# Kernel tuning notes

Hardware: AMD Instinct MI355X
Metric: run time of the kernel (lower is better)

Reference implementation:

```python
import jax, jax.numpy as jnp
import numpy as np

ITERS = 4
LN_EPS = 1e-5


def build_grid(H, W):
    # standard uORF grid in [-1, 1], shape (H, W, 2), last dim = (x, y)
    x = jnp.linspace(-1.0 + 1.0 / W, 1.0 - 1.0 / W, W)
    y = jnp.linspace(-1.0 + 1.0 / H, 1.0 - 1.0 / H, H)
    yy, xx = jnp.meshgrid(y, x, indexing='ij')
    return jnp.stack([xx, yy], axis=-1)


def ln(x, g, b):
    m = jnp.mean(x, axis=-1, keepdims=True)
    v = jnp.var(x, axis=-1, keepdims=True)
    return (x - m) * jax.lax.rsqrt(v + LN_EPS) * g + b


def setup_inputs():
    key = jax.random.key(0)
    ks = jax.random.split(key, 16)
    B, H, W, C, K, Ds = 4, 64, 64, 256, 5, 256
    s = 0.02
    inp = {
        'feat': jax.random.normal(ks[0], (B, H, W, C), jnp.float32),
        'mask': (jax.random.uniform(ks[1], (K, 1, H, W)) > 0.5).astype(jnp.float32),
        'noise': jax.random.normal(ks[2], (B, K, Ds), jnp.float32),
        'slots_mu': jax.random.normal(ks[3], (1, 1, Ds), jnp.float32),
        'slots_logsigma': jax.random.normal(ks[4], (1, 1, Ds), jnp.float32) * s,
        'norm_g': jnp.ones((C,), jnp.float32), 'norm_b': jnp.zeros((C,), jnp.float32),
        'grid_W': jax.random.normal(ks[5], (C, 4), jnp.float32) * s,
        'grid_b': jnp.zeros((C,), jnp.float32),
        'k_W': jax.random.normal(ks[6], (C, C), jnp.float32) * s,
        'v_W': jax.random.normal(ks[7], (C, C), jnp.float32) * s,
        'mlp_g': jnp.ones((C,), jnp.float32), 'mlp_b': jnp.zeros((C,), jnp.float32),
        'mlp_W': jax.random.normal(ks[8], (Ds, C), jnp.float32) * s,
        'mlp_bias': jnp.zeros((Ds,), jnp.float32),
        'q_g': jnp.ones((Ds,), jnp.float32), 'q_b': jnp.zeros((Ds,), jnp.float32),
        'q_W': jax.random.normal(ks[9], (Ds, Ds), jnp.float32) * s,
        'gru_Wih': jax.random.normal(ks[10], (3 * Ds, Ds), jnp.float32) * s,
        'gru_Whh': jax.random.normal(ks[11], (3 * Ds, Ds), jnp.float32) * s,
        'gru_bih': jnp.zeros((3 * Ds,), jnp.float32),
        'gru_bhh': jnp.zeros((3 * Ds,), jnp.float32),
        'res_g': jnp.ones((Ds,), jnp.float32), 'res_b': jnp.zeros((Ds,), jnp.float32),
        'res_W': jax.random.normal(ks[12], (Ds, Ds), jnp.float32) * s,
        'res_bias': jnp.zeros((Ds,), jnp.float32),
    }
    return inp


def reference(feat, mask, noise, slots_mu, slots_logsigma, norm_g, norm_b,
              grid_W, grid_b, k_W, v_W, mlp_g, mlp_b, mlp_W, mlp_bias,
              q_g, q_b, q_W, gru_Wih, gru_Whh, gru_bih, gru_bhh,
              res_g, res_b, res_W, res_bias):
    B, H, W, C = feat.shape
    K = mask.shape[0]
    N = H * W
    Ds = slots_mu.shape[-1]
    scale = Ds ** -0.5

    grid = build_grid(H, W)                                   # (H, W, 2)
    # foreground positions: mask-weighted mean of grid -> (K, 2)
    g = jnp.transpose(grid, (2, 0, 1))[None]                  # (1, 2, H, W)
    fg_pos = jnp.sum(g * mask, axis=(2, 3)) / (jnp.sum(mask, axis=(2, 3)) + 1e-5)
    fg_pos = jnp.broadcast_to(fg_pos[None], (B, K, 2))        # (B, K, 2)

    feat_n = ln(feat.reshape(B, N, C), norm_g, norm_b)        # (B, N, C)
    mask_flat = mask.reshape(K, N)
    slot = slots_mu + jnp.exp(slots_logsigma) * noise         # (B, K, Ds)

    # k, v with relative position embedding; fg_pos never changes in-loop,
    # so compute once (the original recomputes the same values each iter).
    rel = grid.reshape(1, 1, N, 2) - fg_pos[:, :, None, :]    # (B, K, N, 2)
    rel4 = jnp.concatenate([rel, -rel], axis=-1)              # (B, K, N, 4)
    ge = rel4 @ grid_W.T + grid_b                             # (B, K, N, C)
    kbase = feat_n @ k_W.T                                    # (B, N, C)
    vbase = feat_n @ v_W.T
    kk = ln(kbase[:, None] + ge, mlp_g, mlp_b) @ mlp_W.T + mlp_bias  # (B,K,N,Ds)
    vv = ln(vbase[:, None] + ge, mlp_g, mlp_b) @ mlp_W.T + mlp_bias

    attn_vis = None
    for _ in range(ITERS):
        slot_prev = slot
        q = ln(slot, q_g, q_b) @ q_W.T                        # (B, K, Ds)
        attn = jnp.einsum('bkd,bknd->bkn', q, kk) * scale
        attn = jnp.where(mask_flat[None] == 0, -1e9, attn)
        attn = jax.nn.softmax(attn, axis=-1)                  # (B, K, N)
        upd = jnp.einsum('bkn,bknd->bkd', attn, vv)           # (B, K, Ds)
        # torch GRUCell
        x = upd.reshape(-1, Ds)
        h = slot.reshape(-1, Ds)
        gi = x @ gru_Wih.T + gru_bih
        gh = h @ gru_Whh.T + gru_bhh
        ir, iz, inn = jnp.split(gi, 3, axis=-1)
        hr, hz, hn = jnp.split(gh, 3, axis=-1)
        r = jax.nn.sigmoid(ir + hr)
        z = jax.nn.sigmoid(iz + hz)
        n = jnp.tanh(inn + r * hn)
        hnew = ((1.0 - z) * n + z * h).reshape(B, K, Ds)
        slot = (ln(hnew, res_g, res_b) @ res_W.T + res_bias) + slot_prev
        amin = attn.min(axis=-1, keepdims=True)
        amax = attn.max(axis=-1, keepdims=True)
        attn_vis = (attn - amin) / (amax - amin + 1e-5)
    return slot, fg_pos, attn_vis
```

## Files before the change

### kernel.cpp

```cpp
#include <hip/hip_runtime.h>
#include <math.h>

typedef unsigned short u16;
typedef unsigned int   u32;
typedef short bf8v __attribute__((ext_vector_type(8)));
typedef float f4v  __attribute__((ext_vector_type(4)));

static constexpr int B_=4, C_=256, K_=5, D_=256, N_=4096, IT_=4;
static constexpr float EPS_=1e-5f;
static constexpr int P_WQ0=0, P_WR0=16, P_WIH0=32, P_WHH0=80,
                     P_CPK=128, P_CPV=160, P_CPG=192,
                     P_MISC=224, P_UQ=225, P_FG0=226, P_GRID=231;

__device__ __forceinline__ float bf2f(u16 u){ u32 x=((u32)u)<<16; float f; __builtin_memcpy(&f,&x,4); return f; }
__device__ __forceinline__ float bflo(u32 u){ u32 x=u<<16; float f; __builtin_memcpy(&f,&x,4); return f; }
__device__ __forceinline__ float bfhi(u32 u){ u32 x=u&0xffff0000u; float f; __builtin_memcpy(&f,&x,4); return f; }
__device__ __forceinline__ u16 f2bf(float f){ u32 x; __builtin_memcpy(&x,&f,4); u32 r=x+0x7fffu+((x>>16)&1u); return (u16)(r>>16); }
__device__ __forceinline__ float ldin(const void* p, size_t i, int f){
  return f ? ((const float*)p)[i] : bf2f(((const u16*)p)[i]);
}
__device__ __forceinline__ void stout(void* p, size_t i, float v, int f){
  if (f) ((float*)p)[i]=v; else ((u16*)p)[i]=f2bf(v);
}
__device__ __forceinline__ int sw16(int row,int col){
  return row*256 + ((((col>>3)^(row&7))<<3) | (col&7));
}

__device__ __forceinline__ void breduce4(float&a,float&b,float&c,float&d,float* red){
  #pragma unroll
  for(int o=32;o>0;o>>=1){
    a+=__shfl_down(a,o,64); b+=__shfl_down(b,o,64);
    c+=__shfl_down(c,o,64); d+=__shfl_down(d,o,64);
  }
  int w=threadIdx.x>>6;
  __syncthreads();
  if((threadIdx.x&63)==0){ red[w]=a; red[4+w]=b; red[8+w]=c; red[12+w]=d; }
  __syncthreads();
  a=red[0]+red[1]+red[2]+red[3];
  b=red[4]+red[5]+red[6]+red[7];
  c=red[8]+red[9]+red[10]+red[11];
  d=red[12]+red[13]+red[14]+red[15];
}
__device__ __forceinline__ void breduce4_16(float&a,float&b,float&c,float&d,float* red){
  #pragma unroll
  for(int o=32;o>0;o>>=1){
    a+=__shfl_down(a,o,64); b+=__shfl_down(b,o,64);
    c+=__shfl_down(c,o,64); d+=__shfl_down(d,o,64);
  }
  int w=threadIdx.x>>6;
  __syncthreads();
  if((threadIdx.x&63)==0){ red[w]=a; red[16+w]=b; red[32+w]=c; red[48+w]=d; }
  __syncthreads();
  a=0;b=0;c=0;d=0;
  #pragma unroll
  for(int i=0;i<16;++i){ a+=red[i]; b+=red[16+i]; c+=red[32+i]; d+=red[48+i]; }
}

__device__ __forceinline__ int probe_f(const void* feat, float* red){
  const u32* p=(const u32*)feat;
  int t=threadIdx.x; int bad=0;
  #pragma unroll
  for(int s=0;s<8;++s){
    u32 wd=p[t+s*256];
    float lo=bf2f((u16)(wd&0xffffu));
    if(!(fabsf(lo)<1e6f)) bad++;
  }
  float bb=(float)bad, z1=0,z2=0,z3=0;
  breduce4(bb,z1,z2,z3,red);
  return (bb>=16.f)?1:0;
}

__global__ void prep1_kernel(const void* feat,
    const void* kW, const void* vW, const void* mW, const void* qW, const void* rW,
    const void* Wih, const void* Whh, const void* mu, const void* lsig, const void* noise,
    const void* gW, const void* gb_, const void* mg,
    const void* mb_, const void* mbias, const void* mask,
    int* flag, float* WqT, float* WrT, float* WihT, float* WhhT,
    float* slot, float* gvec,
    u16* Wkb, u16* Wvb, u16* Wgb,
    float* Uvec, float* Qs, float* fg, void* out)
{
  __shared__ float redp[16];
  __shared__ float tile[64][65];
  int bid=blockIdx.x;
  int t=threadIdx.x;
  int f=probe_f(feat, redp);
  if(bid==0 && t==0) *flag=f;
  __syncthreads();
  if(bid<P_CPK){
    const void* src; float* dst; int OS; int b2;
    if(bid<P_WR0){ src=qW; dst=WqT; OS=256; b2=bid; }
    else if(bid<P_WIH0){ src=rW; dst=WrT; OS=256; b2=bid-P_WR0; }
    else if(bid<P_WHH0){ src=Wih; dst=WihT; OS=768; b2=bid-P_WIH0; }
    else { src=Whh; dst=WhhT; OS=768; b2=bid-P_WHH0; }
    int r0=(b2>>2)*64, c0=(b2&3)*64;
    int lane=t&63, wv=t>>6;
    #pragma unroll
    for(int it=0;it<16;++it){
      int i=wv*16+it;
      tile[i][lane]=ldin(src,(size_t)(r0+i)*256+c0+lane,f);
    }
    __syncthreads();
    #pragma unroll
    for(int it=0;it<16;++it){
      int i=wv*16+it;
      dst[(size_t)(c0+i)*OS + r0 + lane] = tile[lane][i];
    }
    return;
  }
  if(bid<P_MISC){
    int b2=bid-P_CPK;
    int which=b2>>5;
    int base=(b2&31)*2048;
    if(which==0){
      #pragma unroll
      for(int s=0;s<8;++s){ int e=base+s*256+t; Wkb[e]=f2bf(ldin(kW,e,f)); }
    } else if(which==1){
      #pragma unroll
      for(int s=0;s<8;++s){ int e=base+s*256+t; Wvb[e]=f2bf(ldin(vW,e,f)); }
    } else {
      #pragma unroll
      for(int s=0;s<8;++s){ int e=base+s*256+t; int c=e&255; Wgb[e]=f2bf(ldin(mg,c,f)*ldin(mW,e,f)); }
    }
    return;
  }
  if(bid==P_MISC){
    #pragma unroll
    for(int s=0;s<20;++s){ int e=s*256+t; int d=e&255;
      slot[e]=ldin(mu,d,f)+expf(ldin(lsig,d,f))*ldin(noise,e,f); }
    #pragma unroll
    for(int s=0;s<3;++s){ int e=s*256+t;
      int c=e&255, sel=e>>8;
      float v;
      if(sel==0)      v=ldin(gW,c*4+0,f)-ldin(gW,c*4+2,f);
      else if(sel==1) v=ldin(gW,c*4+1,f)-ldin(gW,c*4+3,f);
      else            v=ldin(gb_,c,f);
      gvec[e]=v;
    }
    return;
  }
  __shared__ float s_a[256], s_b[256], s_c[256];
  if(bid==P_UQ){
    s_a[t]=ldin(gW,t*4+0,f)-ldin(gW,t*4+2,f);
    s_b[t]=ldin(gW,t*4+1,f)-ldin(gW,t*4+3,f);
    s_c[t]=ldin(gb_,t,f);
    __syncthreads();
    float u1=0,u2=0,u3=0,gw=0,bw=0;
    #pragma unroll 8
    for(int c=0;c<256;++c){
      float mwv=ldin(mW,(size_t)t*256+c,f);
      float wg=ldin(mg,c,f)*mwv;
      u1+=s_a[c]*wg; u2+=s_b[c]*wg; u3+=s_c[c]*wg; gw+=wg;
      bw+=ldin(mb_,c,f)*mwv;
    }
    Uvec[t]=u1; Uvec[256+t]=u2; Uvec[512+t]=u3; Uvec[768+t]=gw;
    Uvec[1024+t]=bw+ldin(mbias,t,f);
    float a=s_a[t], b=s_b[t], cc=s_c[t];
    float s0=a*a,s1=b*b,s2=cc*cc,s3=a*b; breduce4(s0,s1,s2,s3,redp);
    float s4=a*cc,s5=b*cc,s6=a,s7=b;     breduce4(s4,s5,s6,s7,redp);
    float s8=cc,z1=0,z2=0,z3=0;          breduce4(s8,z1,z2,z3,redp);
    if(t==0){
      Qs[0]=s0; Qs[1]=s1; Qs[2]=s2; Qs[3]=s3; Qs[4]=s4; Qs[5]=s5;
      Qs[6]=s6*(1.f/256.f); Qs[7]=s7*(1.f/256.f); Qs[8]=s8*(1.f/256.f);
    }
  } else {
    int k=bid-P_FG0;
    float sx=0,sy=0,sm=0;
    for(int s=0;s<16;++s){
      int p=t+s*256;
      float m=ldin(mask,(size_t)k*N_+p,f);
      int i=p>>6, j=p&63;
      float x=(2*j+1)*(1.0f/64.0f)-1.0f;
      float y=(2*i+1)*(1.0f/64.0f)-1.0f;
      sx+=x*m; sy+=y*m; sm+=m;
    }
    float d=0;
    breduce4(sx,sy,sm,d,redp);
    if(t==0){
      float inv=1.0f/(sm+1e-5f);
      float fx=sx*inv, fy=sy*inv;
      fg[k*2]=fx; fg[k*2+1]=fy;
      for(int b=0;b<B_;++b){
        stout(out, 5120+(b*K_+k)*2+0, fx, f);
        stout(out, 5120+(b*K_+k)*2+1, fy, f);
      }
    }
  }
}

__global__ void __launch_bounds__(512,2) base_kernel(const int* flag, const void* feat, const void* ng, const void* nb,
    const u16* Wkb, const u16* Wvb, const u16* Wgb, const float* gvec,
    float* scal, u16* PkT, u16* Pvb,
    const float* slot, const void* qg, const void* qb_, const float* WqT,
    float* qbuf)
{
  extern __shared__ u16 smem[];
  u16* bufA = smem;
  u16* bufB = smem + 16384;
  int t=threadIdx.x, f=*flag;
  if(blockIdx.x>=256){
    float* Lq =(float*)smem;
    float* pp =(float*)smem+256;
    float* red=(float*)smem+768;
    int bk=blockIdx.x-256;
    int tt=t&255, hh=t>>8, w=t>>6;
    float x=slot[bk*256+tt];
    float s=x, s2=x*x;
    #pragma unroll
    for(int o=32;o>0;o>>=1){ s+=__shfl_down(s,o,64); s2+=__shfl_down(s2,o,64); }
    if((t&63)==0){ red[w]=s; red[8+w]=s2; }
    __syncthreads();
    s=0; s2=0;
    #pragma unroll
    for(int i=0;i<8;++i){ s+=red[i]; s2+=red[8+i]; }
    float m=s*(1.f/512.f), v=s2*(1.f/512.f)-m*m;
    float lq=(x-m)*rsqrtf(v+EPS_)*ldin(qg,tt,f)+ldin(qb_,tt,f);
    if(hh==0) Lq[tt]=lq;
    __syncthreads();
    float acc=0; int cb=hh*128;
    #pragma unroll 8
    for(int cc=0;cc<128;++cc){ int c=cb+cc; acc+=Lq[c]*WqT[(size_t)c*256+tt]; }
    pp[hh*256+tt]=acc;
    __syncthreads();
    if(hh==0) qbuf[bk*256+tt]=pp[tt]+pp[256+tt];
    return;
  }
  int w=t>>6, l=t&63;
  int quad=l>>4, m=l&15;
  int row0=blockIdx.x*64;
  {
    float g0=ldin(ng,4*l+0,f), g1=ldin(ng,4*l+1,f), g2=ldin(ng,4*l+2,f), g3=ldin(ng,4*l+3,f);
    float b0=ldin(nb,4*l+0,f), b1=ldin(nb,4*l+1,f), b2=ldin(nb,4*l+2,f), b3=ldin(nb,4*l+3,f);
    #pragma unroll
    for(int r8=0;r8<8;++r8){
      int row=8*w+r8;
      float x0,x1,x2,x3;
      if(f){
        float4 v4=((const float4*)feat)[(size_t)(row0+row)*64+l];
        x0=v4.x; x1=v4.y; x2=v4.z; x3=v4.w;
      } else {
        ushort4 uu=((const ushort4*)feat)[(size_t)(row0+row)*64+l];
        x0=bf2f(uu.x); x1=bf2f(uu.y); x2=bf2f(uu.z); x3=bf2f(uu.w);
      }
      float s=x0+x1+x2+x3, s2=x0*x0+x1*x1+x2*x2+x3*x3;
      #pragma unroll
      for(int o=32;o>0;o>>=1){ s+=__shfl_xor(s,o,64); s2+=__shfl_xor(s2,o,64); }
      float mm=s*(1.f/256.f), inv=rsqrtf(s2*(1.f/256.f)-mm*mm+EPS_);
      ushort4 o4=make_ushort4(f2bf((x0-mm)*inv*g0+b0), f2bf((x1-mm)*inv*g1+b1),
                              f2bf((x2-mm)*inv*g2+b2), f2bf((x3-mm)*inv*g3+b3));
      *(ushort4*)&bufA[sw16(row,4*l)]=o4;
    }
  }
  __syncthreads();
  {
    f4v ack[4][2], acv[4][2];
    #pragma unroll
    for(int rt=0;rt<4;++rt)
      #pragma unroll
      for(int i=0;i<2;++i){ ack[rt][i]=(f4v){0.f,0.f,0.f,0.f}; acv[rt][i]=(f4v){0.f,0.f,0.f,0.f}; }
    #pragma unroll
    for(int kk=0;kk<8;++kk){
      int kcol=kk*32+quad*8;
      bf8v af[4];
      #pragma unroll
      for(int rt=0;rt<4;++rt) af[rt]=*(bf8v*)&bufA[sw16(rt*16+m,kcol)];
      #pragma unroll
      for(int i=0;i<2;++i){
        int n=w*32+16*i+m;
        bf8v bk=*(const bf8v*)(Wkb+(size_t)n*256+kcol);
        bf8v bv=*(const bf8v*)(Wvb+(size_t)n*256+kcol);
        #pragma unroll
        for(int rt=0;rt<4;++rt){
          ack[rt][i]=__builtin_amdgcn_mfma_f32_16x16x32_bf16(af[rt],bk,ack[rt][i],0,0,0);
          acv[rt][i]=__builtin_amdgcn_mfma_f32_16x16x32_bf16(af[rt],bv,acv[rt][i],0,0,0);
        }
      }
    }
    #pragma unroll
    for(int rt=0;rt<4;++rt)
      #pragma unroll
      for(int i=0;i<2;++i){
        int n=w*32+16*i+m;
        #pragma unroll
        for(int r=0;r<4;++r)
          bufB[sw16(rt*16+quad*4+r,n)]=f2bf(ack[rt][i][r]);
      }
    __syncthreads();
    #pragma unroll
    for(int rt=0;rt<4;++rt)
      #pragma unroll
      for(int i=0;i<2;++i){
        int n=w*32+16*i+m;
        #pragma unroll
        for(int r=0;r<4;++r)
          bufA[sw16(rt*16+quad*4+r,n)]=f2bf(acv[rt][i][r]);
      }
  }
  __syncthreads();
  {
    float gA0=gvec[l], gA1=gvec[l+64], gA2=gvec[l+128], gA3=gvec[l+192];
    float gB0=gvec[256+l], gB1=gvec[256+l+64], gB2=gvec[256+l+128], gB3=gvec[256+l+192];
    float gC0=gvec[512+l], gC1=gvec[512+l+64], gC2=gvec[512+l+128], gC3=gvec[512+l+192];
    for(int r8=0;r8<8;++r8){
      int row=8*w+r8;
      float k0=bf2f(bufB[sw16(row,l)]),     k1=bf2f(bufB[sw16(row,l+64)]),
            k2=bf2f(bufB[sw16(row,l+128)]), k3=bf2f(bufB[sw16(row,l+192)]);
      float x0=bf2f(bufA[sw16(row,l)]),     x1=bf2f(bufA[sw16(row,l+64)]),
            x2=bf2f(bufA[sw16(row,l+128)]), x3=bf2f(bufA[sw16(row,l+192)]);
      float v0=k0+k1+k2+k3;
      float v1=k0*k0+k1*k1+k2*k2+k3*k3;
      float v2=k0*gA0+k1*gA1+k2*gA2+k3*gA3;
      float v3=k0*gB0+k1*gB1+k2*gB2+k3*gB3;
      float v4=k0*gC0+k1*gC1+k2*gC2+k3*gC3;
      float v5=x0+x1+x2+x3;
      float v6=x0*x0+x1*x1+x2*x2+x3*x3;
      float v7=x0*gA0+x1*gA1+x2*gA2+x3*gA3;
      float v8=x0*gB0+x1*gB1+x2*gB2+x3*gB3;
      float v9=x0*gC0+x1*gC1+x2*gC2+x3*gC3;
      #pragma unroll
      for(int o=32;o>0;o>>=1){
        v0+=__shfl_down(v0,o,64); v1+=__shfl_down(v1,o,64); v2+=__shfl_down(v2,o,64);
        v3+=__shfl_down(v3,o,64); v4+=__shfl_down(v4,o,64); v5+=__shfl_down(v5,o,64);
        v6+=__shfl_down(v6,o,64); v7+=__shfl_down(v7,o,64); v8+=__shfl_down(v8,o,64);
        v9+=__shfl_down(v9,o,64);
      }
      if(l==0){
        float* sc=scal+(size_t)(row0+row)*10;
        sc[0]=v0; sc[1]=v1; sc[2]=v2; sc[3]=v3; sc[4]=v4;
        sc[5]=v5; sc[6]=v6; sc[7]=v7; sc[8]=v8; sc[9]=v9;
      }
    }
  }
  {
    f4v apk[4][2], apv[4][2];
    #pragma unroll
    for(int rt=0;rt<4;++rt)
      #pragma unroll
      for(int i=0;i<2;++i){ apk[rt][i]=(f4v){0.f,0.f,0.f,0.f}; apv[rt][i]=(f4v){0.f,0.f,0.f,0.f}; }
    #pragma unroll
    for(int kk=0;kk<8;++kk){
      int kcol=kk*32+quad*8;
      bf8v afk[4], afv[4];
      #pragma unroll
      for(int rt=0;rt<4;++rt){
        afk[rt]=*(bf8v*)&bufB[sw16(rt*16+m,kcol)];
        afv[rt]=*(bf8v*)&bufA[sw16(rt*16+m,kcol)];
      }
      #pragma unroll
      for(int i=0;i<2;++i){
        int n=w*32+16*i+m;
        bf8v bg=*(const bf8v*)(Wgb+(size_t)n*256+kcol);
        #pragma unroll
        for(int rt=0;rt<4;++rt){
          apk[rt][i]=__builtin_amdgcn_mfma_f32_16x16x32_bf16(afk[rt],bg,apk[rt][i],0,0,0);
          apv[rt][i]=__builtin_amdgcn_mfma_f32_16x16x32_bf16(afv[rt],bg,apv[rt][i],0,0,0);
        }
      }
    }
    #pragma unroll
    for(int rt=0;rt<4;++rt)
      #pragma unroll
      for(int i=0;i<2;++i){
        int d=w*32+16*i+m;
        *(ushort4*)(PkT+(size_t)d*16384+row0+rt*16+quad*4)=
          make_ushort4(f2bf(apk[rt][i][0]),f2bf(apk[rt][i][1]),f2bf(apk[rt][i][2]),f2bf(apk[rt][i][3]));
      }
    __syncthreads();
    #pragma unroll
    for(int rt=0;rt<4;++rt)
      #pragma unroll
      for(int i=0;i<2;++i){
        int d=w*32+16*i+m;
        #pragma unroll
        for(int r=0;r<4;++r)
          bufB[sw16(rt*16+quad*4+r,d)]=f2bf(apv[rt][i][r]);
      }
  }
  __syncthreads();
  #pragma unroll
  for(int r8=0;r8<8;++r8){
    int row=8*w+r8;
    ushort4 s4=*(ushort4*)&bufB[sw16(row,4*l)];
    *(ushort4*)(Pvb+(size_t)(row0+row)*256+4*l)=s4;
  }
}

__global__ void __launch_bounds__(512) attn_kernel(const int* flag, const float* qbuf, const u16* PkT,
    const float* scal, const float* Qs, const float* Uvec, const float* fg, const void* mask,
    const u16* Pvb, float* logits, float* pmax, float* psum, float* updpart, float* sscp,
    int store_lg)
{
  __shared__ float q5[1280];
  __shared__ float un[10240];
  __shared__ float lgs[320], ivs[320], mvs[320];
  __shared__ float qs5[40], fgs[10], Qss[9], MSl[5];
  __shared__ float sred[8][5][4];
  int tid=threadIdx.x, f=*flag;
  int b=blockIdx.x>>6, ch=blockIdx.x&63;
  int w=tid>>6, l=tid&63;
  int n0=ch<<6;
  for(int p=tid;p<1280;p+=512) q5[p]=qbuf[(size_t)b*1280+p];
  if(tid<10) fgs[tid]=fg[tid];
  if(tid<9)  Qss[tid]=Qs[tid];
  __syncthreads();
  for(int p=w;p<25;p+=8){
    int k=p/5, j=p%5;
    float s=q5[k*256+l]*Uvec[j*256+l]+q5[k*256+l+64]*Uvec[j*256+l+64]
           +q5[k*256+l+128]*Uvec[j*256+l+128]+q5[k*256+l+192]*Uvec[j*256+l+192];
    #pragma unroll
    for(int o=32;o>0;o>>=1) s+=__shfl_xor(s,o,64);
    if(l==0) qs5[k*8+j]=s;
  }
  {
    int n=n0+l; size_t row=(size_t)b*N_+n;
    float dk0=0,dk1=0,dk2=0,dk3=0,dk4=0;
    int cbase=w*32;
    #pragma unroll 8
    for(int cc=0;cc<32;++cc){
      int c=cbase+cc;
      float pv=bf2f(PkT[(size_t)c*16384+row]);
      dk0+=pv*q5[c]; dk1+=pv*q5[256+c]; dk2+=pv*q5[512+c];
      dk3+=pv*q5[768+c]; dk4+=pv*q5[1024+c];
    }
    un[(w*5+0)*64+l]=dk0; un[(w*5+1)*64+l]=dk1; un[(w*5+2)*64+l]=dk2;
    un[(w*5+3)*64+l]=dk3; un[(w*5+4)*64+l]=dk4;
  }
  __syncthreads();
  if(tid<320){
    int k=tid>>6, nl=tid&63;
    float dot=0;
    #pragma unroll
    for(int j=0;j<8;++j) dot+=un[(j*5+k)*64+nl];
    int n2=n0+nl; size_t row2=(size_t)b*N_+n2;
    const float* sc=scal+row2*10;
    float rx=(2*(n2&63)+1)*(1.f/64.f)-1.f-fgs[2*k];
    float ry=(2*(n2>>6)+1)*(1.f/64.f)-1.f-fgs[2*k+1];
    float qge=rx*rx*Qss[0]+ry*ry*Qss[1]+Qss[2]+2.f*(rx*ry*Qss[3]+rx*Qss[4]+ry*Qss[5]);
    float mk=sc[0]*(1.f/256.f)+rx*Qss[6]+ry*Qss[7]+Qss[8];
    float sxk=sc[1]+2.f*(rx*sc[2]+ry*sc[3]+sc[4])+qge;
    float invK=rsqrtf(sxk*(1.f/256.f)-mk*mk+EPS_);
    float lg=invK*(dot+rx*qs5[k*8+0]+ry*qs5[k*8+1]+qs5[k*8+2]-mk*qs5[k*8+3])+qs5[k*8+4];
    float mval=ldin(mask,(size_t)k*N_+n2,f);
    lg=(mval==0.f)? -1e9f : lg*0.0625f;
    if(store_lg) logits[((size_t)(b*5+k))*N_+n2]=lg;
    lgs[tid]=lg;
    float mv=sc[5]*(1.f/256.f)+rx*Qss[6]+ry*Qss[7]+Qss[8];
    float sxv=sc[6]+2.f*(rx*sc[7]+ry*sc[8]+sc[9])+qge;
    mvs[tid]=mv;
    ivs[tid]=rsqrtf(sxv*(1.f/256.f)-mv*mv+EPS_);
  }
  __syncthreads();
  if(tid<64){
    #pragma unroll
    for(int k=0;k<5;++k){
      float v=lgs[k*64+tid];
      float M=v;
      #pragma unroll
      for(int o=32;o>0;o>>=1) M=fmaxf(M,__shfl_xor(M,o,64));
      float e=expf(v-M);
      #pragma unroll
      for(int o=32;o>0;o>>=1) e+=__shfl_xor(e,o,64);
      if(tid==0){ pmax[((size_t)(b*64+ch))*5+k]=M; psum[((size_t)(b*64+ch))*5+k]=e; MSl[k]=M; }
    }
  }
  __syncthreads();
  {
    float acc[5][4]={{0}};
    float swx[5]={0,0,0,0,0}, swy[5]={0,0,0,0,0}, sw[5]={0,0,0,0,0}, swm[5]={0,0,0,0,0};
    #pragma unroll 2
    for(int rr=0;rr<8;++rr){
      int nl=w*8+rr; int n2=n0+nl;
      size_t row=(size_t)b*N_+n2;
      uint2 pu=*(const uint2*)(Pvb+row*256+l*4);
      float px=bflo(pu.x), py=bfhi(pu.x), pz=bflo(pu.y), pw=bfhi(pu.y);
      int jx=n2&63, iy=n2>>6;
      #pragma unroll
      for(int k=0;k<5;++k){
        float wgt=expf(lgs[k*64+nl]-MSl[k])*ivs[k*64+nl];
        float rx=(2*jx+1)*(1.f/64.f)-1.f-fgs[2*k];
        float ry=(2*iy+1)*(1.f/64.f)-1.f-fgs[2*k+1];
        acc[k][0]+=wgt*px; acc[k][1]+=wgt*py; acc[k][2]+=wgt*pz; acc[k][3]+=wgt*pw;
        sw[k]+=wgt; swx[k]+=wgt*rx; swy[k]+=wgt*ry; swm[k]+=wgt*mvs[k*64+nl];
      }
    }
    #pragma unroll
    for(int k=0;k<5;++k)
      *(float4*)&un[(w*5+k)*256+l*4]=make_float4(acc[k][0],acc[k][1],acc[k][2],acc[k][3]);
    if(l==0){
      #pragma unroll
      for(int k=0;k<5;++k){ sred[w][k][0]=swx[k]; sred[w][k][1]=swy[k];
                            sred[w][k][2]=sw[k];  sred[w][k][3]=swm[k]; }
    }
  }
  __syncthreads();
  for(int p=tid;p<1280;p+=512){
    int k=p>>8, d=p&255;
    float v=0;
    #pragma unroll
    for(int j=0;j<8;++j) v+=un[(j*5+k)*256+d];
    updpart[((size_t)blockIdx.x*5+k)*256+d]=v;
  }
  if(tid<20){
    int kk=tid>>2, j=tid&3;
    float s=0;
    #pragma unroll
    for(int jj=0;jj<8;++jj) s+=sred[jj][kk][j];
    sscp[((size_t)blockIdx.x*5+kk)*4+j]=s;
  }
}

__global__ void __launch_bounds__(1024) gru_kernel(const int* flag, float* slot, const float* updpart,
    const float* sscp, const float* Uvec, const float* pmax, const float* psum, const float* logits,
    const float* WihT, const float* WhhT, const void* bih, const void* bhh,
    const void* rg, const void* rb_, const float* WrT, const void* rbias,
    const void* qg, const void* qb_, const float* WqT, float* qbuf,
    int do_vis, void* out)
{
  __shared__ float u[256], h[256], sn[256];
  __shared__ float part[4][6][256];
  __shared__ float red[64];
  __shared__ float cvec[4];
  __shared__ float fch[64];
  __shared__ float MSg[2];
  int tid=threadIdx.x, t=tid&255, g=tid>>8;
  int blk=blockIdx.x;
  int f=*flag;
  if(blk>=20){
    if(!do_vis) return;
    int bk2=blk-20, k2=bk2%K_, b2=bk2/K_;
    if(tid<64){
      float pm=pmax[((size_t)(b2*64+tid))*5+k2];
      float ps=psum[((size_t)(b2*64+tid))*5+k2];
      float M=pm;
      #pragma unroll
      for(int o=32;o>0;o>>=1) M=fmaxf(M,__shfl_xor(M,o,64));
      float e=ps*expf(pm-M);
      #pragma unroll
      for(int o=32;o>0;o>>=1) e+=__shfl_xor(e,o,64);
      if(tid==0){ MSg[0]=M; MSg[1]=1.0f/e; }
    }
    __syncthreads();
    float M=MSg[0], Sinv=MSg[1];
    float a[4]; float mn=1e30f, mx=-1e30f;
    #pragma unroll
    for(int s=0;s<4;++s){
      a[s]=expf(logits[(size_t)bk2*N_+tid+s*1024]-M)*Sinv;
      mn=fminf(mn,a[s]); mx=fmaxf(mx,a[s]);
    }
    #pragma unroll
    for(int o=32;o>0;o>>=1){ mn=fminf(mn,__shfl_down(mn,o,64)); mx=fmaxf(mx,__shfl_down(mx,o,64)); }
    int wv=tid>>6;
    __syncthreads();
    if((tid&63)==0){ red[wv]=mn; red[16+wv]=mx; }
    __syncthreads();
    mn=1e30f; mx=-1e30f;
    #pragma unroll
    for(int i=0;i<16;++i){ mn=fminf(mn,red[i]); mx=fmaxf(mx,red[16+i]); }
    float inv=1.0f/(mx-mn+1e-5f);
    #pragma unroll
    for(int s=0;s<4;++s) stout(out, 5160+(size_t)bk2*N_+tid+s*1024, (a[s]-mn)*inv, f);
    return;
  }
  int bk=blk, k=bk%K_, b=bk/K_;
  if(tid<64){
    float pm=pmax[((size_t)(b*64+tid))*5+k];
    float ps=psum[((size_t)(b*64+tid))*5+k];
    float M=pm;
    #pragma unroll
    for(int o=32;o>0;o>>=1) M=fmaxf(M,__shfl_xor(M,o,64));
    float fc=expf(pm-M);
    fch[tid]=fc;
    float e=ps*fc;
    #pragma unroll
    for(int o=32;o>0;o>>=1) e+=__shfl_xor(e,o,64);
    if(tid==0){ MSg[0]=M; MSg[1]=1.0f/e; }
  }
  __syncthreads();
  float Sinv=MSg[1];
  float ua=0;
  {
    int ch0=g*16;
    #pragma unroll 4
    for(int ci=0;ci<16;++ci){ int ch=ch0+ci; ua += fch[ch]*updpart[(((size_t)(b*64+ch))*5+k)*256+t]; }
  }
  part[g][0][t]=ua;
  if(t<4){
    float s=0;
    #pragma unroll 4
    for(int ci=0;ci<16;++ci){ int ch=g*16+ci; s += fch[ch]*sscp[(((size_t)(b*64+ch))*5+k)*4+t]; }
    part[g][1][t]=s;
  }
  __syncthreads();
  if(g==0 && t<4) cvec[t]=part[0][1][t]+part[1][1][t]+part[2][1][t]+part[3][1][t];
  __syncthreads();
  if(g==0){
    float uu=part[0][0][t]+part[1][0][t]+part[2][0][t]+part[3][0][t];
    u[t]=(uu+cvec[0]*Uvec[t]+cvec[1]*Uvec[256+t]+cvec[2]*Uvec[512+t]-cvec[3]*Uvec[768+t])*Sinv
         +Uvec[1024+t];
    h[t]=slot[bk*256+t];
  }
  __syncthreads();
  float p0=0,p1=0,p2=0,p3=0,p4=0,p5=0;
  int c0=g*64;
  #pragma unroll 8
  for(int cc=0;cc<64;++cc){
    int c=c0+cc;
    float uc=u[c], hc=h[c];
    const float* wi=WihT+(size_t)c*768+t;
    const float* wh=WhhT+(size_t)c*768+t;
    p0+=uc*wi[0]; p1+=uc*wi[256]; p2+=uc*wi[512];
    p3+=hc*wh[0]; p4+=hc*wh[256]; p5+=hc*wh[512];
  }
  part[g][0][t]=p0; part[g][1][t]=p1; part[g][2][t]=p2;
  part[g][3][t]=p3; part[g][4][t]=p4; part[g][5][t]=p5;
  __syncthreads();
  float hn=0;
  if(g==0){
    float gi0=ldin(bih,t,f)+part[0][0][t]+part[1][0][t]+part[2][0][t]+part[3][0][t];
    float gi1=ldin(bih,256+t,f)+part[0][1][t]+part[1][1][t]+part[2][1][t]+part[3][1][t];
    float gi2=ldin(bih,512+t,f)+part[0][2][t]+part[1][2][t]+part[2][2][t]+part[3][2][t];
    float gh0=ldin(bhh,t,f)+part[0][3][t]+part[1][3][t]+part[2][3][t]+part[3][3][t];
    float gh1=ldin(bhh,256+t,f)+part[0][4][t]+part[1][4][t]+part[2][4][t]+part[3][4][t];
    float gh2=ldin(bhh,512+t,f)+part[0][5][t]+part[1][5][t]+part[2][5][t]+part[3][5][t];
    float r=1.f/(1.f+expf(-(gi0+gh0)));
    float z=1.f/(1.f+expf(-(gi1+gh1)));
    float nn=tanhf(gi2+r*gh2);
    hn=(1.f-z)*nn+z*h[t];
  }
  float s=hn, sq=hn*hn, za=0, zb=0;
  breduce4_16(s,sq,za,zb,red);
  if(g==0){
    float m=s*(1.f/256.f), var=sq*(1.f/256.f)-m*m;
    u[t]=(hn-m)*rsqrtf(var+EPS_)*ldin(rg,t,f)+ldin(rb_,t,f);
  }
  __syncthreads();
  float pr=0;
  #pragma unroll 8
  for(int cc=0;cc<64;++cc){ int c=c0+cc; pr+=u[c]*WrT[(size_t)c*256+t]; }
  part[g][0][t]=pr;
  __syncthreads();
  if(g==0){
    float acc=ldin(rbias,t,f)+h[t]+part[0][0][t]+part[1][0][t]+part[2][0][t]+part[3][0][t];
    slot[bk*256+t]=acc;
    stout(out, (size_t)bk*256+t, acc, f);
    sn[t]=acc;
  }
  __syncthreads();
  float xs=(g==0)? sn[t]:0.f;
  float xq=xs*xs, zc=0, zd=0;
  breduce4_16(xs,xq,zc,zd,red);
  if(g==0){
    float m=xs*(1.f/256.f), var=xq*(1.f/256.f)-m*m;
    u[t]=(sn[t]-m)*rsqrtf(var+EPS_)*ldin(qg,t,f)+ldin(qb_,t,f);
  }
  __syncthreads();
  float pq=0;
  #pragma unroll 8
  for(int cc=0;cc<64;++cc){ int c=c0+cc; pq+=u[c]*WqT[(size_t)c*256+t]; }
  part[g][0][t]=pq;
  __syncthreads();
  if(g==0){
    float qv=part[0][0][t]+part[1][0][t]+part[2][0][t]+part[3][0][t];
    qbuf[bk*256+t]=qv;
  }
}

extern "C" void kernel_launch(void* const* d_in, const int* in_sizes, int n_in,
                              void* d_out, int out_size, void* d_ws, size_t ws_size,
                              hipStream_t stream)
{
  const void* feat =d_in[0];  const void* mask =d_in[1];  const void* noise=d_in[2];
  const void* mu   =d_in[3];  const void* lsig =d_in[4];  const void* ng   =d_in[5];
  const void* nb   =d_in[6];  const void* gW   =d_in[7];  const void* gb_  =d_in[8];
  const void* kW   =d_in[9];  const void* vW   =d_in[10]; const void* mg   =d_in[11];
  const void* mb_  =d_in[12]; const void* mW   =d_in[13]; const void* mbias=d_in[14];
  const void* qg   =d_in[15]; const void* qb_  =d_in[16]; const void* qW   =d_in[17];
  const void* Wih  =d_in[18]; const void* Whh  =d_in[19]; const void* bih  =d_in[20];
  const void* bhh  =d_in[21]; const void* rg   =d_in[22]; const void* rb_  =d_in[23];
  const void* rW   =d_in[24]; const void* rbias=d_in[25];

  char* p=(char*)d_ws;
  auto alloc=[&](size_t bytes)->char*{ char* r=p; p+=(bytes+255)&~(size_t)255; return r; };
  int*   flag   =(int*)  alloc(256);
  float* fg     =(float*)alloc(64);
  float* slot   =(float*)alloc(5120*4);
  float* qbuf   =(float*)alloc(5120*4);
  float* logits =(float*)alloc((size_t)81920*4);
  float* pmax   =(float*)alloc(1280*4);
  float* psum   =(float*)alloc(1280*4);
  float* updpart=(float*)alloc((size_t)256*5*256*4);
  float* sscp   =(float*)alloc((size_t)256*5*4*4);
  float* WqT    =(float*)alloc((size_t)65536*4);
  float* WrT    =(float*)alloc((size_t)65536*4);
  float* WihT   =(float*)alloc((size_t)196608*4);
  float* WhhT   =(float*)alloc((size_t)196608*4);
  float* gvec   =(float*)alloc(768*4);
  float* Uvec   =(float*)alloc(1280*4);
  float* Qs     =(float*)alloc(64);
  float* scal   =(float*)alloc((size_t)163840*4);
  u16*   Wkb    =(u16*)  alloc((size_t)65536*2);
  u16*   Wvb    =(u16*)  alloc((size_t)65536*2);
  u16*   Wgb    =(u16*)  alloc((size_t)65536*2);
  u16*   PkT    =(u16*)  alloc((size_t)16384*256*2);
  u16*   Pvb    =(u16*)  alloc((size_t)16384*256*2);

  prep1_kernel<<<P_GRID,256,0,stream>>>(feat,kW,vW,mW,qW,rW,Wih,Whh,mu,lsig,noise,gW,gb_,mg,
                                        mb_,mbias,mask,
                                        flag,WqT,WrT,WihT,WhhT,slot,gvec,Wkb,Wvb,Wgb,
                                        Uvec,Qs,fg,d_out);
  base_kernel<<<276,512,65536,stream>>>(flag,feat,ng,nb,Wkb,Wvb,Wgb,gvec,scal,PkT,Pvb,
                                        slot,qg,qb_,WqT,qbuf);
  for(int it=0; it<IT_; ++it){
    attn_kernel<<<B_*64,512,0,stream>>>(flag,qbuf,PkT,scal,Qs,Uvec,fg,mask,Pvb,
                                        logits,pmax,psum,updpart,sscp,(it==IT_-1)?1:0);
    int nb_g = (it==IT_-1)? 40 : 20;
    gru_kernel<<<nb_g,1024,0,stream>>>(flag,slot,updpart,sscp,Uvec,pmax,psum,logits,
                                       WihT,WhhT,bih,bhh,rg,rb_,WrT,rbias,
                                       qg,qb_,WqT,qbuf,(it==IT_-1)?1:0,d_out);
  }
}
```

Baseline: 366.1 us.

## Move weight transposes into base kernel and read q weights directly

The small-weight transposes (q, res, GRU input/hidden) move out of the prep kernel into extra blocks of the large base kernel, so they overlap with the main projection work and the prep kernel shrinks. The initial q projection now reads the original row-major q weight with vectorised loads instead of waiting on the transposed copy. The Uvec reduction also stages the norm vectors in shared memory and uses vector loads. Extra blocks in the base kernel could compete for CUs with its main tiles.

Measured after the change: 345.8 us. -5.5%, faster.

```diff
diff --git a/kernel.cpp b/kernel.cpp
--- a/kernel.cpp
+++ b/kernel.cpp
@@ -8,9 +8,8 @@
 
 static constexpr int B_=4, C_=256, K_=5, D_=256, N_=4096, IT_=4;
 static constexpr float EPS_=1e-5f;
-static constexpr int P_WQ0=0, P_WR0=16, P_WIH0=32, P_WHH0=80,
-                     P_CPK=128, P_CPV=160, P_CPG=192,
-                     P_MISC=224, P_UQ=225, P_FG0=226, P_GRID=231;
+static constexpr int P0_MISC=96, P0_UQ=97, P0_FG=98, P0_GRID=103;
+static constexpr int BT_QP=256, BT_TR=276, BT_GRID=404;
 
 __device__ __forceinline__ float bf2f(u16 u){ u32 x=((u32)u)<<16; float f; __builtin_memcpy(&f,&x,4); return f; }
 __device__ __forceinline__ float bflo(u32 u){ u32 x=u<<16; float f; __builtin_memcpy(&f,&x,4); return f; }
@@ -70,48 +69,24 @@
   return (bb>=16.f)?1:0;
 }
 
-__global__ void prep1_kernel(const void* feat,
-    const void* kW, const void* vW, const void* mW, const void* qW, const void* rW,
-    const void* Wih, const void* Whh, const void* mu, const void* lsig, const void* noise,
+__global__ void prep0_kernel(const void* feat,
+    const void* kW, const void* vW, const void* mW,
+    const void* mu, const void* lsig, const void* noise,
     const void* gW, const void* gb_, const void* mg,
     const void* mb_, const void* mbias, const void* mask,
-    int* flag, float* WqT, float* WrT, float* WihT, float* WhhT,
-    float* slot, float* gvec,
+    int* flag, float* slot, float* gvec,
     u16* Wkb, u16* Wvb, u16* Wgb,
     float* Uvec, float* Qs, float* fg, void* out)
 {
   __shared__ float redp[16];
-  __shared__ float tile[64][65];
   int bid=blockIdx.x;
   int t=threadIdx.x;
   int f=probe_f(feat, redp);
   if(bid==0 && t==0) *flag=f;
   __syncthreads();
-  if(bid<P_CPK){
-    const void* src; float* dst; int OS; int b2;
-    if(bid<P_WR0){ src=qW; dst=WqT; OS=256; b2=bid; }
-    else if(bid<P_WIH0){ src=rW; dst=WrT; OS=256; b2=bid-P_WR0; }
-    else if(bid<P_WHH0){ src=Wih; dst=WihT; OS=768; b2=bid-P_WIH0; }
-    else { src=Whh; dst=WhhT; OS=768; b2=bid-P_WHH0; }
-    int r0=(b2>>2)*64, c0=(b2&3)*64;
-    int lane=t&63, wv=t>>6;
-    #pragma unroll
-    for(int it=0;it<16;++it){
-      int i=wv*16+it;
-      tile[i][lane]=ldin(src,(size_t)(r0+i)*256+c0+lane,f);
-    }
-    __syncthreads();
-    #pragma unroll
-    for(int it=0;it<16;++it){
-      int i=wv*16+it;
-      dst[(size_t)(c0+i)*OS + r0 + lane] = tile[lane][i];
-    }
-    return;
-  }
-  if(bid<P_MISC){
-    int b2=bid-P_CPK;
-    int which=b2>>5;
-    int base=(b2&31)*2048;
+  if(bid<P0_MISC){
+    int which=bid>>5;
+    int base=(bid&31)*2048;
     if(which==0){
       #pragma unroll
       for(int s=0;s<8;++s){ int e=base+s*256+t; Wkb[e]=f2bf(ldin(kW,e,f)); }
@@ -124,7 +99,7 @@
     }
     return;
   }
-  if(bid==P_MISC){
+  if(bid==P0_MISC){
     #pragma unroll
     for(int s=0;s<20;++s){ int e=s*256+t; int d=e&255;
       slot[e]=ldin(mu,d,f)+expf(ldin(lsig,d,f))*ldin(noise,e,f); }
@@ -140,18 +115,41 @@
     return;
   }
   __shared__ float s_a[256], s_b[256], s_c[256];
-  if(bid==P_UQ){
+  if(bid==P0_UQ){
+    __shared__ float s_mg[256], s_mb[256];
     s_a[t]=ldin(gW,t*4+0,f)-ldin(gW,t*4+2,f);
     s_b[t]=ldin(gW,t*4+1,f)-ldin(gW,t*4+3,f);
     s_c[t]=ldin(gb_,t,f);
+    s_mg[t]=ldin(mg,t,f);
+    s_mb[t]=ldin(mb_,t,f);
     __syncthreads();
     float u1=0,u2=0,u3=0,gw=0,bw=0;
-    #pragma unroll 8
-    for(int c=0;c<256;++c){
-      float mwv=ldin(mW,(size_t)t*256+c,f);
-      float wg=ldin(mg,c,f)*mwv;
-      u1+=s_a[c]*wg; u2+=s_b[c]*wg; u3+=s_c[c]*wg; gw+=wg;
-      bw+=ldin(mb_,c,f)*mwv;
+    if(f){
+      const float4* rp=(const float4*)mW + (size_t)t*64;
+      #pragma unroll 8
+      for(int j=0;j<64;++j){
+        float4 v4=rp[j]; int c=j*4;
+        float m0=v4.x,m1=v4.y,m2=v4.z,m3=v4.w;
+        float w0=s_mg[c]*m0, w1=s_mg[c+1]*m1, w2=s_mg[c+2]*m2, w3=s_mg[c+3]*m3;
+        u1+=s_a[c]*w0+s_a[c+1]*w1+s_a[c+2]*w2+s_a[c+3]*w3;
+        u2+=s_b[c]*w0+s_b[c+1]*w1+s_b[c+2]*w2+s_b[c+3]*w3;
+        u3+=s_c[c]*w0+s_c[c+1]*w1+s_c[c+2]*w2+s_c[c+3]*w3;
+        gw+=w0+w1+w2+w3;
+        bw+=s_mb[c]*m0+s_mb[c+1]*m1+s_mb[c+2]*m2+s_mb[c+3]*m3;
+      }
+    } else {
+      const bf8v* rp=(const bf8v*)((const u16*)mW + (size_t)t*256);
+      #pragma unroll 8
+      for(int j=0;j<32;++j){
+        bf8v v8=rp[j]; int c=j*8;
+        #pragma unroll
+        for(int e=0;e<8;++e){
+          float mwv=bf2f((u16)(unsigned short)v8[e]);
+          float wg=s_mg[c+e]*mwv;
+          u1+=s_a[c+e]*wg; u2+=s_b[c+e]*wg; u3+=s_c[c+e]*wg; gw+=wg;
+          bw+=s_mb[c+e]*mwv;
+        }
+      }
     }
     Uvec[t]=u1; Uvec[256+t]=u2; Uvec[512+t]=u3; Uvec[768+t]=gw;
     Uvec[1024+t]=bw+ldin(mbias,t,f);
@@ -164,8 +162,9 @@
       Qs[6]=s6*(1.f/256.f); Qs[7]=s7*(1.f/256.f); Qs[8]=s8*(1.f/256.f);
     }
   } else {
-    int k=bid-P_FG0;
+    int k=bid-P0_FG;
     float sx=0,sy=0,sm=0;
+    #pragma unroll
     for(int s=0;s<16;++s){
       int p=t+s*256;
       float m=ldin(mask,(size_t)k*N_+p,f);
@@ -191,18 +190,43 @@
 __global__ void __launch_bounds__(512,2) base_kernel(const int* flag, const void* feat, const void* ng, const void* nb,
     const u16* Wkb, const u16* Wvb, const u16* Wgb, const float* gvec,
     float* scal, u16* PkT, u16* Pvb,
-    const float* slot, const void* qg, const void* qb_, const float* WqT,
+    const float* slot, const void* qg, const void* qb_, const void* qW,
+    const void* rW, const void* Wih, const void* Whh,
+    float* WqT, float* WrT, float* WihT, float* WhhT,
     float* qbuf)
 {
   extern __shared__ u16 smem[];
   u16* bufA = smem;
   u16* bufB = smem + 16384;
   int t=threadIdx.x, f=*flag;
-  if(blockIdx.x>=256){
+  if(blockIdx.x>=BT_TR){
+    float (*tile)[65] = (float(*)[65])smem;
+    int b2=blockIdx.x-BT_TR;
+    const void* src; float* dst; int OS;
+    if(b2<16){ src=qW; dst=WqT; OS=256; }
+    else if(b2<32){ src=rW; dst=WrT; OS=256; b2-=16; }
+    else if(b2<80){ src=Wih; dst=WihT; OS=768; b2-=32; }
+    else { src=Whh; dst=WhhT; OS=768; b2-=80; }
+    int r0=(b2>>2)*64, c0=(b2&3)*64;
+    int lane=t&63, wv=t>>6;
+    #pragma unroll
+    for(int it=0;it<8;++it){
+      int i=wv*8+it;
+      tile[i][lane]=ldin(src,(size_t)(r0+i)*256+c0+lane,f);
+    }
+    __syncthreads();
+    #pragma unroll
+    for(int it=0;it<8;++it){
+      int i=wv*8+it;
+      dst[(size_t)(c0+i)*OS + r0 + lane] = tile[lane][i];
+    }
+    return;
+  }
+  if(blockIdx.x>=BT_QP){
     float* Lq =(float*)smem;
     float* pp =(float*)smem+256;
     float* red=(float*)smem+768;
-    int bk=blockIdx.x-256;
+    int bk=blockIdx.x-BT_QP;
     int tt=t&255, hh=t>>8, w=t>>6;
     float x=slot[bk*256+tt];
     float s=x, s2=x*x;
@@ -218,8 +242,22 @@
     if(hh==0) Lq[tt]=lq;
     __syncthreads();
     float acc=0; int cb=hh*128;
-    #pragma unroll 8
-    for(int cc=0;cc<128;++cc){ int c=cb+cc; acc+=Lq[c]*WqT[(size_t)c*256+tt]; }
+    if(f){
+      const float4* rp=(const float4*)qW + ((size_t)tt*256+cb)/4;
+      #pragma unroll 8
+      for(int j=0;j<32;++j){
+        float4 v4=rp[j]; int c=cb+j*4;
+        acc+=Lq[c]*v4.x+Lq[c+1]*v4.y+Lq[c+2]*v4.z+Lq[c+3]*v4.w;
+      }
+    } else {
+      const bf8v* rp=(const bf8v*)((const u16*)qW + (size_t)tt*256+cb);
+      #pragma unroll 8
+      for(int j=0;j<16;++j){
+        bf8v v8=rp[j]; int c=cb+j*8;
+        #pragma unroll
+        for(int e=0;e<8;++e) acc+=Lq[c+e]*bf2f((u16)(unsigned short)v8[e]);
+      }
+    }
     pp[hh*256+tt]=acc;
     __syncthreads();
     if(hh==0) qbuf[bk*256+tt]=pp[tt]+pp[256+tt];
@@ -704,12 +742,13 @@
   u16*   PkT    =(u16*)  alloc((size_t)16384*256*2);
   u16*   Pvb    =(u16*)  alloc((size_t)16384*256*2);
 
-  prep1_kernel<<<P_GRID,256,0,stream>>>(feat,kW,vW,mW,qW,rW,Wih,Whh,mu,lsig,noise,gW,gb_,mg,
-                                        mb_,mbias,mask,
-                                        flag,WqT,WrT,WihT,WhhT,slot,gvec,Wkb,Wvb,Wgb,
-                                        Uvec,Qs,fg,d_out);
-  base_kernel<<<276,512,65536,stream>>>(flag,feat,ng,nb,Wkb,Wvb,Wgb,gvec,scal,PkT,Pvb,
-                                        slot,qg,qb_,WqT,qbuf);
+  prep0_kernel<<<P0_GRID,256,0,stream>>>(feat,kW,vW,mW,mu,lsig,noise,gW,gb_,mg,
+                                         mb_,mbias,mask,
+                                         flag,slot,gvec,Wkb,Wvb,Wgb,
+                                         Uvec,Qs,fg,d_out);
+  base_kernel<<<BT_GRID,512,65536,stream>>>(flag,feat,ng,nb,Wkb,Wvb,Wgb,gvec,scal,PkT,Pvb,
+                                            slot,qg,qb_,qW,rW,Wih,Whh,
+                                            WqT,WrT,WihT,WhhT,qbuf);
   for(int it=0; it<IT_; ++it){
     attn_kernel<<<B_*64,512,0,stream>>>(flag,qbuf,PkT,scal,Qs,Uvec,fg,mask,Pvb,
                                         logits,pmax,psum,updpart,sscp,(it==IT_-1)?1:0);
```
